# Performance work log

Hardware: AMD Instinct MI355X
Metric: run time of the kernel (lower is better)

Reference implementation:

```python
import jax, jax.numpy as jnp
import numpy as np

B, I, DI, O, DO = 256, 1152, 8, 10, 16
ROUTING_ITERS = 3


def squash(s):
    # squash along last dim (out_capsule_dim); keepdims version of the
    # module's intended math: v = s * |s|^2 / (1+|s|^2) / |s|
    sq = jnp.sum(s * s, axis=-1, keepdims=True)
    return s * sq / (1.0 + sq) / jnp.sqrt(sq)


def setup_inputs() -> dict:
    key = jax.random.key(0)
    k1, k2 = jax.random.split(key)
    x = jax.random.normal(k1, (B, I, DI), dtype=jnp.float32)
    stdv = 1.0 / np.sqrt(I)
    W = jax.random.uniform(k2, (I, O, DO, DI), dtype=jnp.float32,
                           minval=-stdv, maxval=stdv)
    return {"x": x, "W": W}


def reference(x, W):
    # u_hat[b,i,o,d] = W[i,o,d,k] @ x[b,i,k]
    u_hat = jnp.einsum('iodk,bik->biod', W, x)  # [B, I, O, DO]
    u_det = jax.lax.stop_gradient(u_hat)
    b_ij = jnp.zeros((B, I, O), dtype=u_hat.dtype)
    v = None
    for it in range(ROUTING_ITERS):
        c = jax.nn.softmax(b_ij, axis=2)              # softmax over out caps
        uh = u_hat if it == ROUTING_ITERS - 1 else u_det
        s = jnp.einsum('bio,biod->bod', c, uh)        # [B, O, DO]
        v = squash(s)
        if it < ROUTING_ITERS - 1:
            b_ij = b_ij + jnp.einsum('biod,bod->bio', u_det, v)
    return v  # [B, O, DO]
```

## Files before the change

kernel.cpp:

```cpp
#include <hip/hip_runtime.h>
#include <hip/hip_fp16.h>
#include <math.h>


constexpr int Bc  = 256;
constexpr int Ic  = 1152;
constexpr int Oc  = 10;
constexpr int DOc = 16;
constexpr int ODc = 160;
constexpr int ITILES = 72;

__device__ __forceinline__ float dpp16_sum(float v) {
    int s;
    s = __builtin_amdgcn_update_dpp(0, __float_as_int(v), 0xB1, 0xF, 0xF, true);
    v += __int_as_float(s);
    s = __builtin_amdgcn_update_dpp(0, __float_as_int(v), 0x4E, 0xF, 0xF, true);
    v += __int_as_float(s);
    s = __builtin_amdgcn_update_dpp(0, __float_as_int(v), 0x124, 0xF, 0xF, true);
    v += __int_as_float(s);
    s = __builtin_amdgcn_update_dpp(0, __float_as_int(v), 0x128, 0xF, 0xF, true);
    v += __int_as_float(s);
    return v;
}

__device__ __forceinline__ unsigned int pack_h2(float a, float b) {
    __half2 h = __floats2half2_rn(a, b);
    unsigned int u;
    __builtin_memcpy(&u, &h, 4);
    return u;
}

__device__ __forceinline__ float2 unpack_h2(unsigned int u) {
    __half2 h;
    __builtin_memcpy(&h, &u, 4);
    return __half22float2(h);
}

__global__ __launch_bounds__(256, 4) void k_uhat(const float* __restrict__ x,
                                                 const float* __restrict__ W,
                                                 uint4* __restrict__ ws4,
                                                 unsigned int* __restrict__ ws1,
                                                 float* __restrict__ partial) {
    const int bx    = blockIdx.x;
    const int itile = bx % ITILES;
    const int btile = bx / ITILES;
    const int t     = threadIdx.x;
    const int d     = t & 15;
    const int il    = t >> 4;
    const int w     = t >> 6;
    const int i     = itile * 16 + il;
    const int b0    = btile * 16;

    __shared__ __align__(16) float xs[16 * 128];
    __shared__ __align__(16) float pacc[4 * 8 * ODc];

#pragma unroll
    for (int j = 0; j < 2; ++j) {
        int e  = t + j * 256;
        int bb = e >> 5;
        int r  = e & 31;
        ((float4*)xs)[e] =
            ((const float4*)(x + (size_t)(b0 + bb) * (Ic * 8) + itile * 128))[r];
    }

    float4 wr[20];
    {
        const float4* wp = (const float4*)(W + (((size_t)i * Oc) * DOc + d) * 8);
#pragma unroll
        for (int o = 0; o < Oc; ++o) {
            wr[2 * o]     = wp[o * 32];
            wr[2 * o + 1] = wp[o * 32 + 1];
        }
    }
    __syncthreads();

    const int chg   = i >> 6;
    const int t_pos = (i & 63) * 16 + d;

#pragma unroll 1
    for (int half = 0; half < 2; ++half) {
#pragma unroll 1
        for (int bb8 = 0; bb8 < 8; ++bb8) {
            const int bb = half * 8 + bb8;
            const int b  = b0 + bb;
            const float4 xa = *((const float4*)(xs + bb * 128 + il * 8));
            const float4 xb = *((const float4*)(xs + bb * 128 + il * 8 + 4));
            float u[Oc];
#pragma unroll
            for (int o = 0; o < Oc; ++o) {
                float4 w0 = wr[2 * o], w1 = wr[2 * o + 1];
                u[o] = w0.x * xa.x + w0.y * xa.y + w0.z * xa.z + w0.w * xa.w +
                       w1.x * xb.x + w1.y * xb.y + w1.z * xb.z + w1.w * xb.w;
            }
            const size_t idx = ((size_t)b * 18 + chg) * 1024 + t_pos;
            ws4[idx] = make_uint4(pack_h2(u[0], u[1]), pack_h2(u[2], u[3]),
                                  pack_h2(u[4], u[5]), pack_h2(u[6], u[7]));
            ws1[idx] = pack_h2(u[8], u[9]);
#pragma unroll
            for (int o = 0; o < Oc; ++o) {
                float a = u[o];
                a += __shfl_xor(a, 16);
                a += __shfl_xor(a, 32);
                if ((t & 63) < 16) pacc[(w * 8 + bb8) * ODc + o * 16 + d] = a;
            }
        }
        __syncthreads();
#pragma unroll
        for (int j = 0; j < 5; ++j) {
            int e = t + j * 256;
            float s = pacc[e] + pacc[1280 + e] + pacc[2560 + e] + pacc[3840 + e];
            partial[(size_t)itile * (Bc * ODc) + (b0 + half * 8) * ODc + e] = s;
        }
        __syncthreads();
    }
}

template <int PASS>
__global__ __launch_bounds__(1024, 8) void k_route(const uint4* __restrict__ ws4,
                                                   const unsigned int* __restrict__ ws1,
                                                   const float* __restrict__ partial,
                                                   const float* __restrict__ sprev,
                                                   float* __restrict__ vsumg,
                                                   float* __restrict__ spart) {
    const int bx  = blockIdx.x;
    const int b   = bx >> 1;
    const int h   = bx & 1;
    const int t   = threadIdx.x;
    const int d   = t & 15;
    const int wid = t >> 6;

    __shared__ float vs_s[ODc];
    __shared__ float red4[4 * ODc];
    __shared__ float red[16 * ODc];

    if (PASS == 1) {
        const int team = t >> 8;
        const int tt   = t & 255;
        if (tt < ODc) {
            float s = 0.f;
            const float* pb = partial + (size_t)team * 18 * (Bc * ODc) + b * ODc + tt;
#pragma unroll 6
            for (int p = 0; p < 18; ++p) s += pb[(size_t)p * (Bc * ODc)];
            red4[team * ODc + tt] = s;
        }
        __syncthreads();
        if (t < ODc) {
            float s = (red4[t] + red4[ODc + t] + red4[2 * ODc + t] +
                       red4[3 * ODc + t]) * 0.1f;
            float sq = dpp16_sum(s * s);
            float v = s * (sq / ((1.f + sq) * sqrtf(sq)));
            vs_s[t] = v;
            vsumg[b * ODc + t] = v;
        }
    } else {
        if (t < ODc) {
            float s = sprev[b * ODc + t] + sprev[(size_t)(Bc * ODc) + b * ODc + t];
            float sq = dpp16_sum(s * s);
            float v = s * (sq / ((1.f + sq) * sqrtf(sq)));
            vs_s[t] = vsumg[b * ODc + t] + v;
        }
    }
    __syncthreads();

    float vsr[Oc];
#pragma unroll
    for (int o = 0; o < Oc; ++o) vsr[o] = vs_s[o * 16 + d];
    float acc[Oc];
#pragma unroll
    for (int o = 0; o < Oc; ++o) acc[o] = 0.f;

    const uint4* wb4        = ws4 + ((size_t)b * 18 + h * 9) * 1024 + t;
    const unsigned int* wb1 = ws1 + ((size_t)b * 18 + h * 9) * 1024 + t;

    uint4 curA        = wb4[0];
    unsigned int curB = wb1[0];
#pragma unroll 1
    for (int ch = 0; ch < 9; ++ch) {
        uint4 nxtA;
        unsigned int nxtB;
        if (ch < 8) {
            nxtA = wb4[(ch + 1) * 1024];
            nxtB = wb1[(ch + 1) * 1024];
        }
        float uo[Oc];
        {
            float2 f;
            f = unpack_h2(curA.x); uo[0] = f.x; uo[1] = f.y;
            f = unpack_h2(curA.y); uo[2] = f.x; uo[3] = f.y;
            f = unpack_h2(curA.z); uo[4] = f.x; uo[5] = f.y;
            f = unpack_h2(curA.w); uo[6] = f.x; uo[7] = f.y;
            f = unpack_h2(curB);   uo[8] = f.x; uo[9] = f.y;
        }
        float c[Oc];
#pragma unroll
        for (int o = 0; o < Oc; ++o) c[o] = dpp16_sum(uo[o] * vsr[o]);
        float m = c[0];
#pragma unroll
        for (int o = 1; o < Oc; ++o) m = fmaxf(m, c[o]);
        float se = 0.f;
#pragma unroll
        for (int o = 0; o < Oc; ++o) {
            c[o] = __expf(c[o] - m);
            se += c[o];
        }
        const float inv = 1.f / se;
#pragma unroll
        for (int o = 0; o < Oc; ++o) acc[o] += (c[o] * inv) * uo[o];
        curA = nxtA;
        curB = nxtB;
    }
#pragma unroll
    for (int o = 0; o < Oc; ++o) {
        float a = acc[o];
        a += __shfl_xor(a, 16);
        a += __shfl_xor(a, 32);
        if ((t & 63) < 16) red[wid * ODc + o * 16 + d] = a;
    }
    __syncthreads();
    if (t < ODc) {
        float s = 0.f;
#pragma unroll
        for (int w = 0; w < 16; ++w) s += red[w * ODc + t];
        spart[(size_t)h * (Bc * ODc) + b * ODc + t] = s;
    }
}

__global__ __launch_bounds__(192) void k_final(const float* __restrict__ spart,
                                               float* __restrict__ out) {
    const int b = blockIdx.x;
    const int t = threadIdx.x;
    if (t >= ODc) return;
    float s = spart[b * ODc + t] + spart[(size_t)(Bc * ODc) + b * ODc + t];
    float sq = dpp16_sum(s * s);
    float v = s * (sq / ((1.f + sq) * sqrtf(sq)));
    out[(size_t)b * ODc + t] = v;
}

__global__ void __launch_bounds__(1024, 4)
digitcaps_fallback(const float* __restrict__ x, const float* __restrict__ W,
                   float* __restrict__ out) {
    const int b = blockIdx.x, t = threadIdx.x;
    const int lane = t & 63, wid = t >> 6, d = t & 15, iblk = t >> 4;
    __shared__ __align__(16) float xs[Ic * 8];
    __shared__ __align__(16) float red[16 * ODc];
    __shared__ __align__(16) float svec[ODc], vcur[ODc], vsum[ODc];
    {
        const float4* xg = (const float4*)(x + (size_t)b * (Ic * 8));
        float4* xl = (float4*)xs;
        for (int j = t; j < Ic * 2; j += 1024) xl[j] = xg[j];
    }
    if (t < ODc) vsum[t] = 0.f;
    __syncthreads();
    float acc[Oc], vsr[Oc];
    for (int it = 0; it < 3; ++it) {
#pragma unroll
        for (int o = 0; o < Oc; ++o) { acc[o] = 0.f; vsr[o] = vsum[o * 16 + d]; }
#pragma unroll 1
        for (int chk = 0; chk < 18; ++chk) {
            const int i = chk * 64 + iblk;
            const float4 xa = ((const float4*)(xs + i * 8))[0];
            const float4 xb = ((const float4*)(xs + i * 8))[1];
            const float* wb = W + (((size_t)i * Oc) * DOc + d) * 8;
            float uo[Oc];
#pragma unroll
            for (int o = 0; o < Oc; ++o) {
                const float4* wp = (const float4*)(wb + o * 128);
                float4 w0 = wp[0], w1 = wp[1];
                uo[o] = w0.x * xa.x + w0.y * xa.y + w0.z * xa.z + w0.w * xa.w +
                        w1.x * xb.x + w1.y * xb.y + w1.z * xb.z + w1.w * xb.w;
            }
            float cc[Oc];
            if (it > 0) {
#pragma unroll
                for (int o = 0; o < Oc; ++o) cc[o] = dpp16_sum(uo[o] * vsr[o]);
                float m = cc[0];
#pragma unroll
                for (int o = 1; o < Oc; ++o) m = fmaxf(m, cc[o]);
                float se = 0.f;
#pragma unroll
                for (int o = 0; o < Oc; ++o) { cc[o] = __expf(cc[o] - m); se += cc[o]; }
                float inv = 1.f / se;
#pragma unroll
                for (int o = 0; o < Oc; ++o) acc[o] += cc[o] * inv * uo[o];
            } else {
#pragma unroll
                for (int o = 0; o < Oc; ++o) acc[o] += 0.1f * uo[o];
            }
        }
#pragma unroll
        for (int o = 0; o < Oc; ++o) {
            float a = acc[o];
            a += __shfl_xor(a, 16);
            a += __shfl_xor(a, 32);
            if (lane < 16) red[wid * ODc + o * 16 + lane] = a;
        }
        __syncthreads();
        if (t < ODc) {
            float s = 0.f;
#pragma unroll
            for (int w = 0; w < 16; ++w) s += red[w * ODc + t];
            svec[t] = s;
        }
        __syncthreads();
        if (t < Oc) {
            float sq = 0.f;
#pragma unroll
            for (int dd = 0; dd < DOc; ++dd) sq += svec[t * 16 + dd] * svec[t * 16 + dd];
            float sc = sq / ((1.f + sq) * sqrtf(sq));
#pragma unroll
            for (int dd = 0; dd < DOc; ++dd) {
                float v = svec[t * 16 + dd] * sc;
                vcur[t * 16 + dd] = v;
                vsum[t * 16 + dd] += v;
            }
        }
        __syncthreads();
    }
    if (t < ODc) out[(size_t)b * ODc + t] = vcur[t];
}

extern "C" void kernel_launch(void* const* d_in, const int* in_sizes, int n_in,
                              void* d_out, int out_size, void* d_ws, size_t ws_size,
                              hipStream_t stream) {
    (void)in_sizes; (void)n_in; (void)out_size;
    const float* x = (const float*)d_in[0];
    const float* W = (const float*)d_in[1];
    float* out     = (float*)d_out;

    const size_t WS4_B  = (size_t)Bc * 18 * 1024 * 16;
    const size_t WS1_B  = (size_t)Bc * 18 * 1024 * 4;
    const size_t PART_B = (size_t)ITILES * Bc * ODc * sizeof(float);
    const size_t SP1_B  = (size_t)2 * Bc * ODc * sizeof(float);
    const size_t SP2_B  = (size_t)2 * Bc * ODc * sizeof(float);
    const size_t VSUM_B = (size_t)Bc * ODc * sizeof(float);

    char* p = (char*)d_ws;
    uint4* ws4        = (uint4*)p;                 p += WS4_B;
    unsigned int* ws1 = (unsigned int*)p;          p += WS1_B;
    float* partial    = (float*)p;                 p += PART_B;
    float* spart1     = (float*)p;                 p += SP1_B;
    float* spart2     = (float*)p;                 p += SP2_B;
    float* vsumg      = (float*)p;

    if (ws_size >= WS4_B + WS1_B + PART_B + SP1_B + SP2_B + VSUM_B) {
        hipLaunchKernelGGL(k_uhat, dim3(ITILES * 16), dim3(256), 0, stream,
                           x, W, ws4, ws1, partial);
        hipLaunchKernelGGL((k_route<1>), dim3(512), dim3(1024), 0, stream,
                           ws4, ws1, partial, nullptr, vsumg, spart1);
        hipLaunchKernelGGL((k_route<2>), dim3(512), dim3(1024), 0, stream,
                           ws4, ws1, nullptr, spart1, vsumg, spart2);
        hipLaunchKernelGGL(k_final, dim3(Bc), dim3(192), 0, stream,
                           spart2, out);
    } else {
        hipLaunchKernelGGL(digitcaps_fallback, dim3(Bc), dim3(1024), 0, stream,
                           x, W, out);
    }
}
```

Measured before the change: 151.9 us.

## Relayout u_hat workspace per itile and preload all chunks in routing kernel

The u_hat workspace is reindexed as contiguous per-(batch, itile) 256-element blocks, so each uhat block writes one contiguous span. The routing kernel moves from 512 blocks of 1024 threads to 1024 blocks of 512 threads, splitting each batch into four quarters. Each thread issues all nine chunk loads up front into registers instead of a one-ahead prefetch loop, exposing more memory-level parallelism. This raises register pressure, and the final and next-pass reductions now sum four partials instead of two.

```diff
diff --git a/kernel.cpp b/kernel.cpp
--- a/kernel.cpp
+++ b/kernel.cpp
@@ -74,9 +74,6 @@
     }
     __syncthreads();
 
-    const int chg   = i >> 6;
-    const int t_pos = (i & 63) * 16 + d;
-
 #pragma unroll 1
     for (int half = 0; half < 2; ++half) {
 #pragma unroll 1
@@ -92,7 +89,7 @@
                 u[o] = w0.x * xa.x + w0.y * xa.y + w0.z * xa.z + w0.w * xa.w +
                        w1.x * xb.x + w1.y * xb.y + w1.z * xb.z + w1.w * xb.w;
             }
-            const size_t idx = ((size_t)b * 18 + chg) * 1024 + t_pos;
+            const size_t idx = ((size_t)b * ITILES + itile) * 256 + t;
             ws4[idx] = make_uint4(pack_h2(u[0], u[1]), pack_h2(u[2], u[3]),
                                   pack_h2(u[4], u[5]), pack_h2(u[6], u[7]));
             ws1[idx] = pack_h2(u[8], u[9]);
@@ -116,37 +113,47 @@
 }
 
 template <int PASS>
-__global__ __launch_bounds__(1024, 8) void k_route(const uint4* __restrict__ ws4,
-                                                   const unsigned int* __restrict__ ws1,
-                                                   const float* __restrict__ partial,
-                                                   const float* __restrict__ sprev,
-                                                   float* __restrict__ vsumg,
-                                                   float* __restrict__ spart) {
-    const int bx  = blockIdx.x;
-    const int b   = bx >> 1;
-    const int h   = bx & 1;
-    const int t   = threadIdx.x;
-    const int d   = t & 15;
-    const int wid = t >> 6;
+__global__ __launch_bounds__(512, 4) void k_route(const uint4* __restrict__ ws4,
+                                                  const unsigned int* __restrict__ ws1,
+                                                  const float* __restrict__ partial,
+                                                  const float* __restrict__ sprev,
+                                                  float* __restrict__ vsumg,
+                                                  float* __restrict__ spart) {
+    const int bx   = blockIdx.x;
+    const int b    = bx >> 2;
+    const int q    = bx & 3;
+    const int t    = threadIdx.x;
+    const int d    = t & 15;
+    const int pos  = t & 255;
+    const int team = t >> 8;
+    const int wv   = t >> 6;
 
     __shared__ float vs_s[ODc];
-    __shared__ float red4[4 * ODc];
-    __shared__ float red[16 * ODc];
+    __shared__ float red3[3 * ODc];
+    __shared__ float red[8 * ODc];
+
+    const size_t base = ((size_t)b * ITILES + q * 18 + team * 9) * 256 + pos;
+    uint4 a4[9];
+    unsigned int a1[9];
+#pragma unroll
+    for (int k = 0; k < 9; ++k) a4[k] = ws4[base + k * 256];
+#pragma unroll
+    for (int k = 0; k < 9; ++k) a1[k] = ws1[base + k * 256];
 
     if (PASS == 1) {
-        const int team = t >> 8;
-        const int tt   = t & 255;
-        if (tt < ODc) {
+        if (t < 3 * ODc) {
+            const int tm = t / ODc;
+            const int r  = t - tm * ODc;
             float s = 0.f;
-            const float* pb = partial + (size_t)team * 18 * (Bc * ODc) + b * ODc + tt;
+            const float* pb =
+                partial + (size_t)tm * 24 * (Bc * ODc) + b * ODc + r;
 #pragma unroll 6
-            for (int p = 0; p < 18; ++p) s += pb[(size_t)p * (Bc * ODc)];
-            red4[team * ODc + tt] = s;
+            for (int p = 0; p < 24; ++p) s += pb[(size_t)p * (Bc * ODc)];
+            red3[t] = s;
         }
         __syncthreads();
         if (t < ODc) {
-            float s = (red4[t] + red4[ODc + t] + red4[2 * ODc + t] +
-                       red4[3 * ODc + t]) * 0.1f;
+            float s = (red3[t] + red3[ODc + t] + red3[2 * ODc + t]) * 0.1f;
             float sq = dpp16_sum(s * s);
             float v = s * (sq / ((1.f + sq) * sqrtf(sq)));
             vs_s[t] = v;
@@ -154,7 +161,10 @@
         }
     } else {
         if (t < ODc) {
-            float s = sprev[b * ODc + t] + sprev[(size_t)(Bc * ODc) + b * ODc + t];
+            float s = sprev[b * ODc + t] +
+                      sprev[((size_t)Bc + b) * ODc + t] +
+                      sprev[((size_t)2 * Bc + b) * ODc + t] +
+                      sprev[((size_t)3 * Bc + b) * ODc + t];
             float sq = dpp16_sum(s * s);
             float v = s * (sq / ((1.f + sq) * sqrtf(sq)));
             vs_s[t] = vsumg[b * ODc + t] + v;
@@ -169,27 +179,16 @@
 #pragma unroll
     for (int o = 0; o < Oc; ++o) acc[o] = 0.f;
 
-    const uint4* wb4        = ws4 + ((size_t)b * 18 + h * 9) * 1024 + t;
-    const unsigned int* wb1 = ws1 + ((size_t)b * 18 + h * 9) * 1024 + t;
-
-    uint4 curA        = wb4[0];
-    unsigned int curB = wb1[0];
-#pragma unroll 1
-    for (int ch = 0; ch < 9; ++ch) {
-        uint4 nxtA;
-        unsigned int nxtB;
-        if (ch < 8) {
-            nxtA = wb4[(ch + 1) * 1024];
-            nxtB = wb1[(ch + 1) * 1024];
-        }
+#pragma unroll
+    for (int k = 0; k < 9; ++k) {
         float uo[Oc];
         {
             float2 f;
-            f = unpack_h2(curA.x); uo[0] = f.x; uo[1] = f.y;
-            f = unpack_h2(curA.y); uo[2] = f.x; uo[3] = f.y;
-            f = unpack_h2(curA.z); uo[4] = f.x; uo[5] = f.y;
-            f = unpack_h2(curA.w); uo[6] = f.x; uo[7] = f.y;
-            f = unpack_h2(curB);   uo[8] = f.x; uo[9] = f.y;
+            f = unpack_h2(a4[k].x); uo[0] = f.x; uo[1] = f.y;
+            f = unpack_h2(a4[k].y); uo[2] = f.x; uo[3] = f.y;
+            f = unpack_h2(a4[k].z); uo[4] = f.x; uo[5] = f.y;
+            f = unpack_h2(a4[k].w); uo[6] = f.x; uo[7] = f.y;
+            f = unpack_h2(a1[k]);   uo[8] = f.x; uo[9] = f.y;
         }
         float c[Oc];
 #pragma unroll
@@ -206,22 +205,20 @@
         const float inv = 1.f / se;
 #pragma unroll
         for (int o = 0; o < Oc; ++o) acc[o] += (c[o] * inv) * uo[o];
-        curA = nxtA;
-        curB = nxtB;
     }
 #pragma unroll
     for (int o = 0; o < Oc; ++o) {
         float a = acc[o];
         a += __shfl_xor(a, 16);
         a += __shfl_xor(a, 32);
-        if ((t & 63) < 16) red[wid * ODc + o * 16 + d] = a;
+        if ((t & 63) < 16) red[wv * ODc + o * 16 + d] = a;
     }
     __syncthreads();
     if (t < ODc) {
         float s = 0.f;
 #pragma unroll
-        for (int w = 0; w < 16; ++w) s += red[w * ODc + t];
-        spart[(size_t)h * (Bc * ODc) + b * ODc + t] = s;
+        for (int w = 0; w < 8; ++w) s += red[w * ODc + t];
+        spart[((size_t)q * Bc + b) * ODc + t] = s;
     }
 }
 
@@ -230,7 +227,10 @@
     const int b = blockIdx.x;
     const int t = threadIdx.x;
     if (t >= ODc) return;
-    float s = spart[b * ODc + t] + spart[(size_t)(Bc * ODc) + b * ODc + t];
+    float s = spart[b * ODc + t] +
+              spart[((size_t)Bc + b) * ODc + t] +
+              spart[((size_t)2 * Bc + b) * ODc + t] +
+              spart[((size_t)3 * Bc + b) * ODc + t];
     float sq = dpp16_sum(s * s);
     float v = s * (sq / ((1.f + sq) * sqrtf(sq)));
     out[(size_t)b * ODc + t] = v;
@@ -327,11 +327,11 @@
     const float* W = (const float*)d_in[1];
     float* out     = (float*)d_out;
 
-    const size_t WS4_B  = (size_t)Bc * 18 * 1024 * 16;
-    const size_t WS1_B  = (size_t)Bc * 18 * 1024 * 4;
+    const size_t WS4_B  = (size_t)Bc * ITILES * 256 * 16;
+    const size_t WS1_B  = (size_t)Bc * ITILES * 256 * 4;
     const size_t PART_B = (size_t)ITILES * Bc * ODc * sizeof(float);
-    const size_t SP1_B  = (size_t)2 * Bc * ODc * sizeof(float);
-    const size_t SP2_B  = (size_t)2 * Bc * ODc * sizeof(float);
+    const size_t SP1_B  = (size_t)4 * Bc * ODc * sizeof(float);
+    const size_t SP2_B  = (size_t)4 * Bc * ODc * sizeof(float);
     const size_t VSUM_B = (size_t)Bc * ODc * sizeof(float);
 
     char* p = (char*)d_ws;
@@ -345,9 +345,9 @@
     if (ws_size >= WS4_B + WS1_B + PART_B + SP1_B + SP2_B + VSUM_B) {
         hipLaunchKernelGGL(k_uhat, dim3(ITILES * 16), dim3(256), 0, stream,
                            x, W, ws4, ws1, partial);
-        hipLaunchKernelGGL((k_route<1>), dim3(512), dim3(1024), 0, stream,
+        hipLaunchKernelGGL((k_route<1>), dim3(Bc * 4), dim3(512), 0, stream,
                            ws4, ws1, partial, nullptr, vsumg, spart1);
-        hipLaunchKernelGGL((k_route<2>), dim3(512), dim3(1024), 0, stream,
+        hipLaunchKernelGGL((k_route<2>), dim3(Bc * 4), dim3(512), 0, stream,
                            ws4, ws1, nullptr, spart1, vsumg, spart2);
         hipLaunchKernelGGL(k_final, dim3(Bc), dim3(192), 0, stream,
                            spart2, out);
```

Measured after the change: 217.4 us. 43.1% more time.
